# Performance work log

Hardware: AMD Instinct MI355X
Metric: run time of the kernel (lower is better)

## Reference

```python
import jax, jax.numpy as jnp
import numpy as np

N, F_IN, HID, H1, NG = 50000, 128, 64, 4, 512
E = 800000


def setup_inputs() -> dict:
    key = jax.random.key(0)
    ks = jax.random.split(key, 16)
    x = jax.random.normal(ks[0], (N, F_IN), dtype=jnp.float32)
    edge_index = jax.random.randint(ks[1], (2, E), 0, N, dtype=jnp.int64)
    batch = jnp.sort(jax.random.randint(ks[2], (N,), 0, NG, dtype=jnp.int64))
    s = 0.05
    W1 = jax.random.normal(ks[3], (F_IN, H1 * HID), dtype=jnp.float32) * s
    a_src1 = jax.random.normal(ks[4], (H1, HID), dtype=jnp.float32) * s
    a_dst1 = jax.random.normal(ks[5], (H1, HID), dtype=jnp.float32) * s
    b1 = jnp.zeros((H1 * HID,), dtype=jnp.float32)
    W2 = jax.random.normal(ks[6], (H1 * HID, HID), dtype=jnp.float32) * s
    a_src2 = jax.random.normal(ks[7], (1, HID), dtype=jnp.float32) * s
    a_dst2 = jax.random.normal(ks[8], (1, HID), dtype=jnp.float32) * s
    b2 = jnp.zeros((HID,), dtype=jnp.float32)
    Wc = jax.random.normal(ks[9], (HID, 2), dtype=jnp.float32) * s
    bc = jnp.zeros((2,), dtype=jnp.float32)
    return dict(x=x, edge_index=edge_index, batch=batch, W1=W1, a_src1=a_src1,
                a_dst1=a_dst1, b1=b1, W2=W2, a_src2=a_src2, a_dst2=a_dst2,
                b2=b2, Wc=Wc, bc=bc)


def gat_layer(x, W, a_src, a_dst, bias, src, dst, n):
    # PyG GATConv: h = x @ W per head; e_ij = LeakyReLU(a_src.h_j + a_dst.h_i),
    # softmax over incoming edges of each dst node, then scatter-add aggregate.
    H, D = a_src.shape
    h = (x @ W).reshape(n, H, D)                       # [N,H,D]
    asrc = jnp.einsum('nhd,hd->nh', h, a_src)          # [N,H]
    adst = jnp.einsum('nhd,hd->nh', h, a_dst)
    e = jax.nn.leaky_relu(asrc[src] + adst[dst], 0.2)  # [E,H]
    m = jax.lax.stop_gradient(jax.ops.segment_max(e, dst, num_segments=n))
    p = jnp.exp(e - m[dst])
    s = jax.ops.segment_sum(p, dst, num_segments=n)
    alpha = p / (s[dst] + 1e-16)                       # [E,H]
    out = jax.ops.segment_sum(alpha[:, :, None] * h[src], dst, num_segments=n)
    return out.reshape(n, H * D) + bias


def reference(x, edge_index, batch, W1, a_src1, a_dst1, b1, W2, a_src2, a_dst2, b2, Wc, bc):
    n = x.shape[0]
    loops = jnp.arange(n, dtype=edge_index.dtype)
    src = jnp.concatenate([edge_index[0], loops])  # add self-loops (PyG default)
    dst = jnp.concatenate([edge_index[1], loops])
    h = jax.nn.relu(gat_layer(x, W1, a_src1, a_dst1, b1, src, dst, n))
    h = jax.nn.relu(gat_layer(h, W2, a_src2, a_dst2, b2, src, dst, n))
    # global mean pool over graphs
    ng = NG
    sums = jax.ops.segment_sum(h, batch, num_segments=ng)
    cnts = jax.ops.segment_sum(jnp.ones((n,), h.dtype), batch, num_segments=ng)
    pooled = sums / jnp.maximum(cnts, 1.0)[:, None]
    logits = pooled @ Wc + bc
    return jax.nn.log_softmax(logits, axis=1)
```

## Files before the change

kernel.cpp:

```cpp
#include <hip/hip_runtime.h>
#include <hip/hip_bf16.h>
#include <cstddef>
#include <cstdint>

#define FIN   128
#define HID   64
#define H1    4
#define NGRAPH 512
#define BCAP  8192
#define PREB  512

typedef short bf16x8 __attribute__((ext_vector_type(8)));
typedef float f32x4  __attribute__((ext_vector_type(4)));

#if defined(__has_builtin)
#if __has_builtin(__builtin_amdgcn_cvt_f32_fp8) && __has_builtin(__builtin_amdgcn_cvt_pk_fp8_f32)
#define HAVE_HW_FP8 1
#endif
#endif

__device__ __forceinline__ float wave_reduce_sum(float v) {
  #pragma unroll
  for (int off = 32; off > 0; off >>= 1) v += __shfl_down(v, off, 64);
  return v;
}

__device__ __forceinline__ float leaky02(float x) {
  return x > 0.0f ? x : 0.2f * x;
}

__device__ __forceinline__ unsigned short f2bf(float f) {
  union { float f; unsigned int i; } v; v.f = f;
  unsigned int b = v.i;
  return (unsigned short)((b + 0x7FFFu + ((b >> 16) & 1u)) >> 16);
}

#ifndef HAVE_HW_FP8
__device__ __forceinline__ unsigned char f2fp8_1(float f) {
  unsigned int u = __float_as_uint(f);
  unsigned int s = u >> 31;
  u &= 0x7fffffffu;
  if (u > 0x43e00000u) u = 0x43e00000u;
  unsigned int b = u + (0x0007FFFFu + ((u >> 20) & 1u));
  int e = (int)(b >> 23) - 127;
  unsigned int m = (b >> 20) & 7u;
  unsigned char o;
  if (e < -9) o = 0;
  else if (e < -6) { int sh = -6 - e; o = (unsigned char)((8u | m) >> sh); }
  else if (e > 8) o = 0x7e;
  else o = (unsigned char)(((e + 7) << 3) | m);
  return o | (unsigned char)(s << 7);
}
__device__ __forceinline__ float fp8tof_1(unsigned char b) {
  unsigned int s = b >> 7, e = (b >> 3) & 15u, m = b & 7u;
  float v = (e == 0) ? (float)m * 0.001953125f
                     : (float)(8u + m) * __uint_as_float((117u + e) << 23);
  return s ? -v : v;
}
#endif

__device__ __forceinline__ unsigned char f2fp8(float f) {
#ifdef HAVE_HW_FP8
  return (unsigned char)(__builtin_amdgcn_cvt_pk_fp8_f32(f, f, 0u, false) & 0xffu);
#else
  return f2fp8_1(f);
#endif
}
__device__ __forceinline__ float fp8dec(unsigned int w, int i) {
#ifdef HAVE_HW_FP8
  switch (i) {
    case 0: return __builtin_amdgcn_cvt_f32_fp8(w, 0);
    case 1: return __builtin_amdgcn_cvt_f32_fp8(w, 1);
    case 2: return __builtin_amdgcn_cvt_f32_fp8(w, 2);
    default: return __builtin_amdgcn_cvt_f32_fp8(w, 3);
  }
#else
  return fp8tof_1((unsigned char)((w >> (8 * i)) & 0xffu));
#endif
}

__global__ __launch_bounds__(256)
void pre_kernel(const float* __restrict__ W1, const float* __restrict__ W2,
                unsigned short* __restrict__ W1T, unsigned short* __restrict__ W2T,
                const int* __restrict__ dst, int* __restrict__ bucketCnt,
                const int* __restrict__ batch, int* __restrict__ gstart,
                int* __restrict__ gend, int E, int N, int nbuck) {
  __shared__ int lh[256];
  int tid = threadIdx.x;
  lh[tid] = 0;
  __syncthreads();
  int stride = gridDim.x * 256;
  int t0 = blockIdx.x * 256 + tid;
  for (int i = t0; i < E; i += stride)
    atomicAdd(&lh[dst[i] >> 8], 1);
  for (int i = t0; i < N; i += stride) {
    int g = batch[i];
    if (i == 0 || batch[i - 1] != g) gstart[g] = i;
    if (i == N - 1 || batch[i + 1] != g) gend[g] = i + 1;
  }
  for (int u = t0; u < 256 * 128; u += stride) {
    int n = u >> 7, k = u & 127;
    W1T[u] = f2bf(W1[(size_t)k * 256 + n]);
  }
  for (int u = t0; u < 64 * 256; u += stride) {
    int n = u >> 8, k = u & 255;
    W2T[u] = f2bf(W2[(size_t)k * 64 + n]);
  }
  __syncthreads();
  if (tid < nbuck && lh[tid] > 0) atomicAdd(&bucketCnt[tid], lh[tid]);
}

#define P3K 16
__global__ __launch_bounds__(256)
void bpart_kernel(const int* __restrict__ src, const int* __restrict__ dst,
                  int* __restrict__ bucketFill, unsigned int* __restrict__ bucketBuf,
                  int E, int nbuck) {
  __shared__ int lhist[256];
  __shared__ int lbase[256];
  int tid = threadIdx.x;
  int chunk = 256 * P3K;
  for (int start = blockIdx.x * chunk; start < E; start += gridDim.x * chunk) {
    lhist[tid] = 0;
    __syncthreads();
    int mybuck[P3K]; unsigned int mypack[P3K]; int myrank[P3K];
    #pragma unroll
    for (int k = 0; k < P3K; k++) {
      int i = start + k * 256 + tid;
      if (i < E) {
        int d = dst[i];
        int b = d >> 8;
        mybuck[k] = b;
        mypack[k] = (unsigned int)src[i] | ((unsigned int)(d & 255) << 16);
        myrank[k] = atomicAdd(&lhist[b], 1);
      } else mybuck[k] = -1;
    }
    __syncthreads();
    if (tid < nbuck) lbase[tid] = (lhist[tid] > 0) ? atomicAdd(&bucketFill[tid], lhist[tid]) : 0;
    __syncthreads();
    #pragma unroll
    for (int k = 0; k < P3K; k++) {
      if (mybuck[k] >= 0) {
        int b = mybuck[k];
        int pos = lbase[b] + myrank[k];
        if (pos < BCAP) bucketBuf[((size_t)b << 13) + pos] = mypack[k];
      }
    }
    __syncthreads();
  }
}

__global__ __launch_bounds__(256)
void bbuild_kernel(const unsigned int* __restrict__ bucketBuf, const int* __restrict__ bucketCnt,
                   int* __restrict__ rowstart, int* __restrict__ rowend,
                   unsigned short* __restrict__ csr, int N) {
  __shared__ int ldeg[256];
  __shared__ int lscan[256];
  __shared__ int lfill[256];
  int b = blockIdx.x;
  int tid = threadIdx.x;
  int r0 = b << 13;
  int cnt = bucketCnt[b]; if (cnt > BCAP) cnt = BCAP;
  int nb0 = b << 8;
  ldeg[tid] = 0;
  __syncthreads();
  for (int j = tid; j < cnt; j += 256)
    atomicAdd(&ldeg[bucketBuf[r0 + j] >> 16], 1);
  __syncthreads();
  int v = ldeg[tid];
  lscan[tid] = v;
  __syncthreads();
  for (int off = 1; off < 256; off <<= 1) {
    int u = (tid >= off) ? lscan[tid - off] : 0;
    __syncthreads();
    lscan[tid] += u;
    __syncthreads();
  }
  int excl = lscan[tid] - v;
  lfill[tid] = excl;
  if (nb0 + tid < N) {
    rowstart[nb0 + tid] = r0 + excl;
    rowend[nb0 + tid]   = r0 + excl + v;
  }
  __syncthreads();
  for (int j = tid; j < cnt; j += 256) {
    unsigned int p = bucketBuf[r0 + j];
    int pos = r0 + atomicAdd(&lfill[p >> 16], 1);
    csr[pos] = (unsigned short)(p & 0xffffu);
  }
}

__global__ __launch_bounds__(256)
void gemm1_kernel(const float* __restrict__ X, const unsigned short* __restrict__ W1T,
                  unsigned char* __restrict__ h1f8,
                  const float* __restrict__ a_src, const float* __restrict__ a_dst,
                  float* __restrict__ asv, float* __restrict__ adv, int N) {
  __shared__ unsigned short As[64][136];
  __shared__ unsigned short Bs[256][40];
  int t = threadIdx.x;
  int w = t >> 6, lane = t & 63;
  int quad = lane >> 4, l16 = lane & 15;
  int blockRow = blockIdx.x * 64;

  {
    int node = t >> 2, kp = (t & 3) * 32;
    int gn = blockRow + node; if (gn >= N) gn = N - 1;
    const float4* xp = (const float4*)(X + (size_t)gn * 128 + kp);
    #pragma unroll
    for (int i = 0; i < 4; i++) {
      float4 va = xp[2 * i], vb = xp[2 * i + 1];
      union { unsigned short u[8]; uint4 v; } r;
      r.u[0] = f2bf(va.x); r.u[1] = f2bf(va.y); r.u[2] = f2bf(va.z); r.u[3] = f2bf(va.w);
      r.u[4] = f2bf(vb.x); r.u[5] = f2bf(vb.y); r.u[6] = f2bf(vb.z); r.u[7] = f2bf(vb.w);
      *(uint4*)&As[node][kp + i * 8] = r.v;
    }
  }

  f32x4 acc[4][4];
  #pragma unroll
  for (int i = 0; i < 4; i++)
    #pragma unroll
    for (int j = 0; j < 4; j++) acc[i][j] = (f32x4){0.f, 0.f, 0.f, 0.f};

  for (int kc = 0; kc < FIN; kc += 32) {
    {
      const unsigned short* wp = W1T + (size_t)t * 128 + kc;
      #pragma unroll
      for (int i = 0; i < 4; i++) {
        uint4 v = *(const uint4*)(wp + i * 8);
        *(uint4*)&Bs[t][i * 8] = v;
      }
    }
    __syncthreads();
    bf16x8 af[4], bfr[4];
    #pragma unroll
    for (int mt = 0; mt < 4; mt++)
      af[mt] = *(const bf16x8*)&As[mt * 16 + l16][kc + quad * 8];
    #pragma unroll
    for (int nt = 0; nt < 4; nt++)
      bfr[nt] = *(const bf16x8*)&Bs[w * 64 + nt * 16 + l16][quad * 8];
    #pragma unroll
    for (int mt = 0; mt < 4; mt++)
      #pragma unroll
      for (int nt = 0; nt < 4; nt++)
        acc[mt][nt] = __builtin_amdgcn_mfma_f32_16x16x32_bf16(af[mt], bfr[nt], acc[mt][nt], 0, 0, 0);
    __syncthreads();
  }

  float a_s[4], a_d[4];
  #pragma unroll
  for (int nt = 0; nt < 4; nt++) {
    a_s[nt] = a_src[w * 64 + nt * 16 + l16];
    a_d[nt] = a_dst[w * 64 + nt * 16 + l16];
  }
  #pragma unroll
  for (int mt = 0; mt < 4; mt++) {
    #pragma unroll
    for (int reg = 0; reg < 4; reg++) {
      int node = blockRow + mt * 16 + quad * 4 + reg;
      bool ok = node < N;
      float ps = 0.0f, pd = 0.0f;
      #pragma unroll
      for (int nt = 0; nt < 4; nt++) {
        float v = acc[mt][nt][reg];
        ps = fmaf(v, a_s[nt], ps);
        pd = fmaf(v, a_d[nt], pd);
        if (ok) h1f8[(size_t)node * 256 + w * 64 + nt * 16 + l16] = f2fp8(v);
      }
      #pragma unroll
      for (int off = 8; off > 0; off >>= 1) {
        ps += __shfl_xor(ps, off, 16);
        pd += __shfl_xor(pd, off, 16);
      }
      if (l16 == 0 && ok) {
        asv[(size_t)node * 4 + w] = ps;
        adv[(size_t)node * 4 + w] = pd;
      }
    }
  }
}

__global__ __launch_bounds__(256)
void gemm2_kernel(const unsigned short* __restrict__ out1b, const unsigned short* __restrict__ W2T,
                  unsigned char* __restrict__ h2f8,
                  const float* __restrict__ a_src, const float* __restrict__ a_dst,
                  float* __restrict__ asv, float* __restrict__ adv, int N) {
  __shared__ unsigned short As[64][40];
  __shared__ unsigned short Bs[64][40];
  int t = threadIdx.x;
  int w = t >> 6, lane = t & 63;
  int quad = lane >> 4, l16 = lane & 15;
  int blockRow = blockIdx.x * 64;

  f32x4 acc[4];
  #pragma unroll
  for (int j = 0; j < 4; j++) acc[j] = (f32x4){0.f, 0.f, 0.f, 0.f};

  int nodeS = t >> 2, koff = (t & 3) * 8;
  int gnS = blockRow + nodeS; if (gnS >= N) gnS = N - 1;

  for (int kc = 0; kc < 256; kc += 32) {
    {
      uint4 va = *(const uint4*)(out1b + (size_t)gnS * 256 + kc + koff);
      *(uint4*)&As[nodeS][koff] = va;
      uint4 vb = *(const uint4*)(W2T + (size_t)nodeS * 256 + kc + koff);
      *(uint4*)&Bs[nodeS][koff] = vb;
    }
    __syncthreads();
    bf16x8 af = *(const bf16x8*)&As[w * 16 + l16][quad * 8];
    #pragma unroll
    for (int nt = 0; nt < 4; nt++) {
      bf16x8 bfr = *(const bf16x8*)&Bs[nt * 16 + l16][quad * 8];
      acc[nt] = __builtin_amdgcn_mfma_f32_16x16x32_bf16(af, bfr, acc[nt], 0, 0, 0);
    }
    __syncthreads();
  }

  float a_s[4], a_d[4];
  #pragma unroll
  for (int nt = 0; nt < 4; nt++) {
    a_s[nt] = a_src[nt * 16 + l16];
    a_d[nt] = a_dst[nt * 16 + l16];
  }
  #pragma unroll
  for (int reg = 0; reg < 4; reg++) {
    int node = blockRow + w * 16 + quad * 4 + reg;
    bool ok = node < N;
    float ps = 0.0f, pd = 0.0f;
    #pragma unroll
    for (int nt = 0; nt < 4; nt++) {
      float v = acc[nt][reg];
      ps = fmaf(v, a_s[nt], ps);
      pd = fmaf(v, a_d[nt], pd);
      if (ok) h2f8[(size_t)node * 64 + nt * 16 + l16] = f2fp8(v);
    }
    #pragma unroll
    for (int off = 8; off > 0; off >>= 1) {
      ps += __shfl_xor(ps, off, 16);
      pd += __shfl_xor(pd, off, 16);
    }
    if (l16 == 0 && ok) { asv[node] = ps; adv[node] = pd; }
  }
}

__global__ __launch_bounds__(256)
void agg1_kernel(const unsigned char* __restrict__ h1f8, const int* __restrict__ rowstart,
                 const int* __restrict__ rowend, const unsigned short* __restrict__ csr,
                 const float* __restrict__ asv, const float* __restrict__ adv,
                 const float* __restrict__ b1, unsigned short* __restrict__ out1b, int N) {
  __shared__ int   sbuf[4][64];
  __shared__ float pbuf[4][4][68];
  int wv   = threadIdx.x >> 6;
  int lane = threadIdx.x & 63;
  int n = blockIdx.x * 4 + wv;
  if (n >= N) return;
  int r0 = rowstart[n], r1 = rowend[n];
  float4 ad = *(const float4*)(adv + (size_t)n * 4);
  float4 asn = *(const float4*)(asv + (size_t)n * 4);
  int hsel = lane >> 4;

  float es0 = leaky02(asn.x + ad.x);
  float es1 = leaky02(asn.y + ad.y);
  float es2 = leaky02(asn.z + ad.z);
  float es3 = leaky02(asn.w + ad.w);
  float esel = hsel == 0 ? es0 : (hsel == 1 ? es1 : (hsel == 2 ? es2 : es3));

  float q0 = 0, q1 = 0, q2 = 0, q3 = 0;
  float a0 = 0, a1 = 0, a2 = 0, a3 = 0;

  for (int base = r0; base < r1; base += 64) {
    int j = base + lane;
    int cnt = min(64, r1 - base);
    if (j < r1) {
      int s = csr[j];
      float4 as = *(const float4*)(asv + (size_t)s * 4);
      sbuf[wv][lane] = s;
      float p0 = __expf(leaky02(as.x + ad.x));
      float p1 = __expf(leaky02(as.y + ad.y));
      float p2 = __expf(leaky02(as.z + ad.z));
      float p3 = __expf(leaky02(as.w + ad.w));
      pbuf[wv][0][lane] = p0;
      pbuf[wv][1][lane] = p1;
      pbuf[wv][2][lane] = p2;
      pbuf[wv][3][lane] = p3;
      q0 += p0; q1 += p1; q2 += p2; q3 += p3;
    }
    __threadfence_block();

    int c = 0;
    for (; c + 4 <= cnt; c += 4) {
      int4 sv = *(const int4*)&sbuf[wv][c];
      int sc0 = __builtin_amdgcn_readfirstlane(sv.x);
      int sc1 = __builtin_amdgcn_readfirstlane(sv.y);
      int sc2 = __builtin_amdgcn_readfirstlane(sv.z);
      int sc3 = __builtin_amdgcn_readfirstlane(sv.w);
      unsigned int hw0 = *((const unsigned int*)(h1f8 + ((size_t)sc0 << 8)) + lane);
      unsigned int hw1 = *((const unsigned int*)(h1f8 + ((size_t)sc1 << 8)) + lane);
      unsigned int hw2 = *((const unsigned int*)(h1f8 + ((size_t)sc2 << 8)) + lane);
      unsigned int hw3 = *((const unsigned int*)(h1f8 + ((size_t)sc3 << 8)) + lane);
      float4 pv = *(const float4*)&pbuf[wv][hsel][c];
      a0 = fmaf(pv.x, fp8dec(hw0, 0), a0);
      a1 = fmaf(pv.x, fp8dec(hw0, 1), a1);
      a2 = fmaf(pv.x, fp8dec(hw0, 2), a2);
      a3 = fmaf(pv.x, fp8dec(hw0, 3), a3);
      a0 = fmaf(pv.y, fp8dec(hw1, 0), a0);
      a1 = fmaf(pv.y, fp8dec(hw1, 1), a1);
      a2 = fmaf(pv.y, fp8dec(hw1, 2), a2);
      a3 = fmaf(pv.y, fp8dec(hw1, 3), a3);
      a0 = fmaf(pv.z, fp8dec(hw2, 0), a0);
      a1 = fmaf(pv.z, fp8dec(hw2, 1), a1);
      a2 = fmaf(pv.z, fp8dec(hw2, 2), a2);
      a3 = fmaf(pv.z, fp8dec(hw2, 3), a3);
      a0 = fmaf(pv.w, fp8dec(hw3, 0), a0);
      a1 = fmaf(pv.w, fp8dec(hw3, 1), a1);
      a2 = fmaf(pv.w, fp8dec(hw3, 2), a2);
      a3 = fmaf(pv.w, fp8dec(hw3, 3), a3);
    }
    for (; c < cnt; c++) {
      int sc = __builtin_amdgcn_readfirstlane(sbuf[wv][c]);
      float psel = pbuf[wv][hsel][c];
      unsigned int hw = *((const unsigned int*)(h1f8 + ((size_t)sc << 8)) + lane);
      a0 = fmaf(psel, fp8dec(hw, 0), a0);
      a1 = fmaf(psel, fp8dec(hw, 1), a1);
      a2 = fmaf(psel, fp8dec(hw, 2), a2);
      a3 = fmaf(psel, fp8dec(hw, 3), a3);
    }
    __threadfence_block();
  }

  #pragma unroll
  for (int off = 32; off > 0; off >>= 1) {
    q0 += __shfl_xor(q0, off, 64);
    q1 += __shfl_xor(q1, off, 64);
    q2 += __shfl_xor(q2, off, 64);
    q3 += __shfl_xor(q3, off, 64);
  }
  float ssum = hsel == 0 ? q0 : (hsel == 1 ? q1 : (hsel == 2 ? q2 : q3));

  {
    float psel = __expf(esel);
    ssum += psel;
    unsigned int hw = *((const unsigned int*)(h1f8 + ((size_t)n << 8)) + lane);
    a0 = fmaf(psel, fp8dec(hw, 0), a0);
    a1 = fmaf(psel, fp8dec(hw, 1), a1);
    a2 = fmaf(psel, fp8dec(hw, 2), a2);
    a3 = fmaf(psel, fp8dec(hw, 3), a3);
  }

  float inv = 1.0f / (ssum + 1e-16f);
  int d0 = lane * 4;
  float4 bv = *(const float4*)(b1 + d0);
  float v0 = a0 * inv + bv.x;
  float v1 = a1 * inv + bv.y;
  float v2 = a2 * inv + bv.z;
  float v3 = a3 * inv + bv.w;
  ushort4 o;
  o.x = f2bf(v0 > 0 ? v0 : 0.0f);
  o.y = f2bf(v1 > 0 ? v1 : 0.0f);
  o.z = f2bf(v2 > 0 ? v2 : 0.0f);
  o.w = f2bf(v3 > 0 ? v3 : 0.0f);
  *(ushort4*)(out1b + (size_t)n * 256 + d0) = o;
}

__global__ __launch_bounds__(256)
void agg2_kernel(const unsigned char* __restrict__ h2f8, const int* __restrict__ rowstart,
                 const int* __restrict__ rowend, const unsigned short* __restrict__ csr,
                 const float* __restrict__ asv, const float* __restrict__ adv,
                 const float* __restrict__ b2, float* __restrict__ h2out, int N) {
  __shared__ int   sbuf[4][64];
  __shared__ float pbuf[4][64];
  int wv   = threadIdx.x >> 6;
  int lane = threadIdx.x & 63;
  int quad = lane >> 4, l16 = lane & 15;
  int n = blockIdx.x * 4 + wv;
  if (n >= N) return;
  int r0 = rowstart[n], r1 = rowend[n];
  float ad = adv[n];
  float eself = leaky02(asv[n] + ad);
  float q = 0.0f;
  float a0 = 0, a1 = 0, a2 = 0, a3 = 0;

  for (int base = r0; base < r1; base += 64) {
    int j = base + lane;
    int cnt = min(64, r1 - base);
    if (j < r1) {
      int s = csr[j];
      sbuf[wv][lane] = s;
      float p = __expf(leaky02(asv[s] + ad));
      pbuf[wv][lane] = p;
      q += p;
    }
    __threadfence_block();

    int c = 0;
    for (; c + 8 <= cnt; c += 8) {
      int scA = sbuf[wv][c + quad];
      int scB = sbuf[wv][c + 4 + quad];
      float pA = pbuf[wv][c + quad];
      float pB = pbuf[wv][c + 4 + quad];
      unsigned int hwA = *((const unsigned int*)(h2f8 + ((size_t)scA << 6)) + l16);
      unsigned int hwB = *((const unsigned int*)(h2f8 + ((size_t)scB << 6)) + l16);
      a0 = fmaf(pA, fp8dec(hwA, 0), a0);
      a1 = fmaf(pA, fp8dec(hwA, 1), a1);
      a2 = fmaf(pA, fp8dec(hwA, 2), a2);
      a3 = fmaf(pA, fp8dec(hwA, 3), a3);
      a0 = fmaf(pB, fp8dec(hwB, 0), a0);
      a1 = fmaf(pB, fp8dec(hwB, 1), a1);
      a2 = fmaf(pB, fp8dec(hwB, 2), a2);
      a3 = fmaf(pB, fp8dec(hwB, 3), a3);
    }
    for (; c + 4 <= cnt; c += 4) {
      int sc = sbuf[wv][c + quad];
      float p1 = pbuf[wv][c + quad];
      unsigned int hw = *((const unsigned int*)(h2f8 + ((size_t)sc << 6)) + l16);
      a0 = fmaf(p1, fp8dec(hw, 0), a0);
      a1 = fmaf(p1, fp8dec(hw, 1), a1);
      a2 = fmaf(p1, fp8dec(hw, 2), a2);
      a3 = fmaf(p1, fp8dec(hw, 3), a3);
    }
    int rem = cnt - c;
    if (quad < rem) {
      int sc = sbuf[wv][c + quad];
      float p1 = pbuf[wv][c + quad];
      unsigned int hw = *((const unsigned int*)(h2f8 + ((size_t)sc << 6)) + l16);
      a0 = fmaf(p1, fp8dec(hw, 0), a0);
      a1 = fmaf(p1, fp8dec(hw, 1), a1);
      a2 = fmaf(p1, fp8dec(hw, 2), a2);
      a3 = fmaf(p1, fp8dec(hw, 3), a3);
    }
    __threadfence_block();
  }

  #pragma unroll
  for (int off = 32; off > 0; off >>= 1) q += __shfl_xor(q, off, 64);
  #pragma unroll
  for (int off = 16; off <= 32; off <<= 1) {
    a0 += __shfl_xor(a0, off, 64);
    a1 += __shfl_xor(a1, off, 64);
    a2 += __shfl_xor(a2, off, 64);
    a3 += __shfl_xor(a3, off, 64);
  }
  float ssum = q;

  {
    float p = __expf(eself);
    ssum += p;
    unsigned int hw = *((const unsigned int*)(h2f8 + ((size_t)n << 6)) + l16);
    a0 = fmaf(p, fp8dec(hw, 0), a0);
    a1 = fmaf(p, fp8dec(hw, 1), a1);
    a2 = fmaf(p, fp8dec(hw, 2), a2);
    a3 = fmaf(p, fp8dec(hw, 3), a3);
  }

  if (quad == 0) {
    float inv = 1.0f / (ssum + 1e-16f);
    float4 bv = *(const float4*)(b2 + l16 * 4);
    float4 o;
    float v0 = a0 * inv + bv.x;
    float v1 = a1 * inv + bv.y;
    float v2 = a2 * inv + bv.z;
    float v3 = a3 * inv + bv.w;
    o.x = v0 > 0 ? v0 : 0.0f;
    o.y = v1 > 0 ? v1 : 0.0f;
    o.z = v2 > 0 ? v2 : 0.0f;
    o.w = v3 > 0 ? v3 : 0.0f;
    *(float4*)(h2out + (size_t)n * 64 + l16 * 4) = o;
  }
}

__global__ __launch_bounds__(256)
void pool_kernel(const float* __restrict__ h2, const int* __restrict__ gstart,
                 const int* __restrict__ gend, const float* __restrict__ Wc,
                 const float* __restrict__ bc, float* __restrict__ out) {
  int g = blockIdx.x;
  int w = threadIdx.x >> 6, lane = threadIdx.x & 63;
  int s = gstart[g], e = gend[g];
  float acc = 0.0f;
  for (int n = s + w; n < e; n += 4) acc += h2[(size_t)n * 64 + lane];
  __shared__ float red[4][64];
  red[w][lane] = acc;
  __syncthreads();
  if (w == 0) {
    float v = red[0][lane] + red[1][lane] + red[2][lane] + red[3][lane];
    float pooled = (e > s) ? v / (float)(e - s) : 0.0f;
    float l0 = wave_reduce_sum(pooled * Wc[lane * 2 + 0]);
    float l1 = wave_reduce_sum(pooled * Wc[lane * 2 + 1]);
    if (lane == 0) {
      l0 += bc[0]; l1 += bc[1];
      float mx = fmaxf(l0, l1);
      float lse = mx + logf(__expf(l0 - mx) + __expf(l1 - mx));
      out[g * 2 + 0] = l0 - lse;
      out[g * 2 + 1] = l1 - lse;
    }
  }
}

extern "C" void kernel_launch(void* const* d_in, const int* in_sizes, int n_in,
                              void* d_out, int out_size, void* d_ws, size_t ws_size,
                              hipStream_t stream) {
  const float* x      = (const float*)d_in[0];
  const int*   ei     = (const int*)d_in[1];
  const int*   batch  = (const int*)d_in[2];
  const float* W1     = (const float*)d_in[3];
  const float* a_src1 = (const float*)d_in[4];
  const float* a_dst1 = (const float*)d_in[5];
  const float* b1     = (const float*)d_in[6];
  const float* W2     = (const float*)d_in[7];
  const float* a_src2 = (const float*)d_in[8];
  const float* a_dst2 = (const float*)d_in[9];
  const float* b2     = (const float*)d_in[10];
  const float* Wc     = (const float*)d_in[11];
  const float* bc     = (const float*)d_in[12];
  float* out = (float*)d_out;

  const int N = in_sizes[0] / FIN;
  const int E = in_sizes[1] / 2;
  const int* srcArr = ei;
  const int* dstArr = ei + E;
  const int nbuck = (N + 255) >> 8;

  char* base = (char*)d_ws;
  size_t off = 0;
  auto alloc = [&](size_t bytes) -> void* {
    void* p = base + off;
    off = (off + bytes + 255) & ~(size_t)255;
    return p;
  };
  unsigned short* W1T  = (unsigned short*)alloc((size_t)256 * 128 * 2);
  unsigned short* W2T  = (unsigned short*)alloc((size_t)64 * 256 * 2);
  unsigned char*  h1f8 = (unsigned char*)alloc((size_t)N * 256);
  unsigned short* out1b= (unsigned short*)alloc((size_t)N * 256 * 2);
  unsigned char*  h2f8 = (unsigned char*)alloc((size_t)N * 64);
  float* h2    = (float*)alloc((size_t)N * 64 * 4);
  float* asv1  = (float*)alloc((size_t)N * 4 * 4);
  float* adv1  = (float*)alloc((size_t)N * 4 * 4);
  float* asv2  = (float*)alloc((size_t)N * 4);
  float* adv2  = (float*)alloc((size_t)N * 4);
  int*   bucketCnt = (int*)alloc(256 * 4);
  int*   bucketFill= (int*)alloc(256 * 4);
  int*   gstart= (int*)alloc(NGRAPH * 4);
  int*   gend  = (int*)alloc(NGRAPH * 4);
  size_t zspan = (size_t)((char*)gend + NGRAPH * 4 - (char*)bucketCnt);
  int*   rowstart = (int*)alloc((size_t)N * 4);
  int*   rowend   = (int*)alloc((size_t)N * 4);
  unsigned int* bucketBuf = (unsigned int*)alloc((size_t)nbuck * BCAP * 4);
  unsigned short* csr = (unsigned short*)alloc((size_t)nbuck * BCAP * 2);
  (void)ws_size; (void)n_in; (void)out_size;

  int gridWv = (N + 3) / 4;
  int gridG  = (N + 63) / 64;
  int gridP3 = (E + 256 * P3K - 1) / (256 * P3K);

  hipMemsetAsync(bucketCnt, 0, zspan, stream);
  pre_kernel<<<PREB, 256, 0, stream>>>(W1, W2, W1T, W2T, dstArr, bucketCnt,
                                       batch, gstart, gend, E, N, nbuck);
  bpart_kernel<<<gridP3, 256, 0, stream>>>(srcArr, dstArr, bucketFill, bucketBuf, E, nbuck);
  bbuild_kernel<<<nbuck, 256, 0, stream>>>(bucketBuf, bucketCnt, rowstart, rowend, csr, N);

  gemm1_kernel<<<gridG, 256, 0, stream>>>(x, W1T, h1f8, a_src1, a_dst1, asv1, adv1, N);
  agg1_kernel<<<gridWv, 256, 0, stream>>>(h1f8, rowstart, rowend, csr, asv1, adv1, b1, out1b, N);

  gemm2_kernel<<<gridG, 256, 0, stream>>>(out1b, W2T, h2f8, a_src2, a_dst2, asv2, adv2, N);
  agg2_kernel<<<gridWv, 256, 0, stream>>>(h2f8, rowstart, rowend, csr, asv2, adv2, b2, h2, N);

  pool_kernel<<<NGRAPH, 256, 0, stream>>>(h2, gstart, gend, Wc, bc, out);
}
```

Baseline: 241.0 us.

## Fold pre-pass into bucket partition kernel and unroll agg1 gather by eight

Removes the separate pre_kernel that histogrammed destination buckets, and moves its weight transposes and graph-boundary detection into bpart_kernel. bbuild now takes bucket counts from the atomic fill counters bpart already keeps, so one full read of dst and one launch go away. The agg1 inner gather loop also gets an 8-wide unrolled step ahead of the 4-wide one, putting more independent fp8 row loads in flight. The costs are higher register pressure in agg1 and some extra serial work in every bpart block.

```diff
diff --git a/kernel.cpp b/kernel.cpp
--- a/kernel.cpp
+++ b/kernel.cpp
@@ -8,7 +8,6 @@
 #define H1    4
 #define NGRAPH 512
 #define BCAP  8192
-#define PREB  512
 
 typedef short bf16x8 __attribute__((ext_vector_type(8)));
 typedef float f32x4  __attribute__((ext_vector_type(4)));
@@ -79,45 +78,33 @@
 #endif
 }
 
+#define P3K 16
 __global__ __launch_bounds__(256)
-void pre_kernel(const float* __restrict__ W1, const float* __restrict__ W2,
-                unsigned short* __restrict__ W1T, unsigned short* __restrict__ W2T,
-                const int* __restrict__ dst, int* __restrict__ bucketCnt,
-                const int* __restrict__ batch, int* __restrict__ gstart,
-                int* __restrict__ gend, int E, int N, int nbuck) {
-  __shared__ int lh[256];
+void bpart_kernel(const int* __restrict__ src, const int* __restrict__ dst,
+                  int* __restrict__ bucketFill, unsigned int* __restrict__ bucketBuf,
+                  const float* __restrict__ W1, const float* __restrict__ W2,
+                  unsigned short* __restrict__ W1T, unsigned short* __restrict__ W2T,
+                  const int* __restrict__ batch, int* __restrict__ gstart,
+                  int* __restrict__ gend, int E, int N, int nbuck) {
   int tid = threadIdx.x;
-  lh[tid] = 0;
-  __syncthreads();
   int stride = gridDim.x * 256;
   int t0 = blockIdx.x * 256 + tid;
-  for (int i = t0; i < E; i += stride)
-    atomicAdd(&lh[dst[i] >> 8], 1);
+  for (int u = t0; u < 256 * 128; u += stride) {
+    int n = u >> 7, k = u & 127;
+    W1T[u] = f2bf(W1[(size_t)k * 256 + n]);
+  }
+  for (int u = t0; u < 64 * 256; u += stride) {
+    int n = u >> 8, k = u & 255;
+    W2T[u] = f2bf(W2[(size_t)k * 64 + n]);
+  }
   for (int i = t0; i < N; i += stride) {
     int g = batch[i];
     if (i == 0 || batch[i - 1] != g) gstart[g] = i;
     if (i == N - 1 || batch[i + 1] != g) gend[g] = i + 1;
   }
-  for (int u = t0; u < 256 * 128; u += stride) {
-    int n = u >> 7, k = u & 127;
-    W1T[u] = f2bf(W1[(size_t)k * 256 + n]);
-  }
-  for (int u = t0; u < 64 * 256; u += stride) {
-    int n = u >> 8, k = u & 255;
-    W2T[u] = f2bf(W2[(size_t)k * 64 + n]);
-  }
-  __syncthreads();
-  if (tid < nbuck && lh[tid] > 0) atomicAdd(&bucketCnt[tid], lh[tid]);
-}
-
-#define P3K 16
-__global__ __launch_bounds__(256)
-void bpart_kernel(const int* __restrict__ src, const int* __restrict__ dst,
-                  int* __restrict__ bucketFill, unsigned int* __restrict__ bucketBuf,
-                  int E, int nbuck) {
+
   __shared__ int lhist[256];
   __shared__ int lbase[256];
-  int tid = threadIdx.x;
   int chunk = 256 * P3K;
   for (int start = blockIdx.x * chunk; start < E; start += gridDim.x * chunk) {
     lhist[tid] = 0;
@@ -150,7 +137,7 @@
 }
 
 __global__ __launch_bounds__(256)
-void bbuild_kernel(const unsigned int* __restrict__ bucketBuf, const int* __restrict__ bucketCnt,
+void bbuild_kernel(const unsigned int* __restrict__ bucketBuf, const int* __restrict__ bucketFill,
                    int* __restrict__ rowstart, int* __restrict__ rowend,
                    unsigned short* __restrict__ csr, int N) {
   __shared__ int ldeg[256];
@@ -159,7 +146,7 @@
   int b = blockIdx.x;
   int tid = threadIdx.x;
   int r0 = b << 13;
-  int cnt = bucketCnt[b]; if (cnt > BCAP) cnt = BCAP;
+  int cnt = bucketFill[b]; if (cnt > BCAP) cnt = BCAP;
   int nb0 = b << 8;
   ldeg[tid] = 0;
   __syncthreads();
@@ -387,6 +374,60 @@
     __threadfence_block();
 
     int c = 0;
+    for (; c + 8 <= cnt; c += 8) {
+      int4 sva = *(const int4*)&sbuf[wv][c];
+      int4 svb = *(const int4*)&sbuf[wv][c + 4];
+      int sc0 = __builtin_amdgcn_readfirstlane(sva.x);
+      int sc1 = __builtin_amdgcn_readfirstlane(sva.y);
+      int sc2 = __builtin_amdgcn_readfirstlane(sva.z);
+      int sc3 = __builtin_amdgcn_readfirstlane(sva.w);
+      int sc4 = __builtin_amdgcn_readfirstlane(svb.x);
+      int sc5 = __builtin_amdgcn_readfirstlane(svb.y);
+      int sc6 = __builtin_amdgcn_readfirstlane(svb.z);
+      int sc7 = __builtin_amdgcn_readfirstlane(svb.w);
+      unsigned int hw0 = *((const unsigned int*)(h1f8 + ((size_t)sc0 << 8)) + lane);
+      unsigned int hw1 = *((const unsigned int*)(h1f8 + ((size_t)sc1 << 8)) + lane);
+      unsigned int hw2 = *((const unsigned int*)(h1f8 + ((size_t)sc2 << 8)) + lane);
+      unsigned int hw3 = *((const unsigned int*)(h1f8 + ((size_t)sc3 << 8)) + lane);
+      unsigned int hw4 = *((const unsigned int*)(h1f8 + ((size_t)sc4 << 8)) + lane);
+      unsigned int hw5 = *((const unsigned int*)(h1f8 + ((size_t)sc5 << 8)) + lane);
+      unsigned int hw6 = *((const unsigned int*)(h1f8 + ((size_t)sc6 << 8)) + lane);
+      unsigned int hw7 = *((const unsigned int*)(h1f8 + ((size_t)sc7 << 8)) + lane);
+      float4 pva = *(const float4*)&pbuf[wv][hsel][c];
+      float4 pvb = *(const float4*)&pbuf[wv][hsel][c + 4];
+      a0 = fmaf(pva.x, fp8dec(hw0, 0), a0);
+      a1 = fmaf(pva.x, fp8dec(hw0, 1), a1);
+      a2 = fmaf(pva.x, fp8dec(hw0, 2), a2);
+      a3 = fmaf(pva.x, fp8dec(hw0, 3), a3);
+      a0 = fmaf(pva.y, fp8dec(hw1, 0), a0);
+      a1 = fmaf(pva.y, fp8dec(hw1, 1), a1);
+      a2 = fmaf(pva.y, fp8dec(hw1, 2), a2);
+      a3 = fmaf(pva.y, fp8dec(hw1, 3), a3);
+      a0 = fmaf(pva.z, fp8dec(hw2, 0), a0);
+      a1 = fmaf(pva.z, fp8dec(hw2, 1), a1);
+      a2 = fmaf(pva.z, fp8dec(hw2, 2), a2);
+      a3 = fmaf(pva.z, fp8dec(hw2, 3), a3);
+      a0 = fmaf(pva.w, fp8dec(hw3, 0), a0);
+      a1 = fmaf(pva.w, fp8dec(hw3, 1), a1);
+      a2 = fmaf(pva.w, fp8dec(hw3, 2), a2);
+      a3 = fmaf(pva.w, fp8dec(hw3, 3), a3);
+      a0 = fmaf(pvb.x, fp8dec(hw4, 0), a0);
+      a1 = fmaf(pvb.x, fp8dec(hw4, 1), a1);
+      a2 = fmaf(pvb.x, fp8dec(hw4, 2), a2);
+      a3 = fmaf(pvb.x, fp8dec(hw4, 3), a3);
+      a0 = fmaf(pvb.y, fp8dec(hw5, 0), a0);
+      a1 = fmaf(pvb.y, fp8dec(hw5, 1), a1);
+      a2 = fmaf(pvb.y, fp8dec(hw5, 2), a2);
+      a3 = fmaf(pvb.y, fp8dec(hw5, 3), a3);
+      a0 = fmaf(pvb.z, fp8dec(hw6, 0), a0);
+      a1 = fmaf(pvb.z, fp8dec(hw6, 1), a1);
+      a2 = fmaf(pvb.z, fp8dec(hw6, 2), a2);
+      a3 = fmaf(pvb.z, fp8dec(hw6, 3), a3);
+      a0 = fmaf(pvb.w, fp8dec(hw7, 0), a0);
+      a1 = fmaf(pvb.w, fp8dec(hw7, 1), a1);
+      a2 = fmaf(pvb.w, fp8dec(hw7, 2), a2);
+      a3 = fmaf(pvb.w, fp8dec(hw7, 3), a3);
+    }
     for (; c + 4 <= cnt; c += 4) {
       int4 sv = *(const int4*)&sbuf[wv][c];
       int sc0 = __builtin_amdgcn_readfirstlane(sv.x);
@@ -635,11 +676,10 @@
   float* adv1  = (float*)alloc((size_t)N * 4 * 4);
   float* asv2  = (float*)alloc((size_t)N * 4);
   float* adv2  = (float*)alloc((size_t)N * 4);
-  int*   bucketCnt = (int*)alloc(256 * 4);
   int*   bucketFill= (int*)alloc(256 * 4);
   int*   gstart= (int*)alloc(NGRAPH * 4);
   int*   gend  = (int*)alloc(NGRAPH * 4);
-  size_t zspan = (size_t)((char*)gend + NGRAPH * 4 - (char*)bucketCnt);
+  size_t zspan = (size_t)((char*)gend + NGRAPH * 4 - (char*)bucketFill);
   int*   rowstart = (int*)alloc((size_t)N * 4);
   int*   rowend   = (int*)alloc((size_t)N * 4);
   unsigned int* bucketBuf = (unsigned int*)alloc((size_t)nbuck * BCAP * 4);
@@ -650,11 +690,11 @@
   int gridG  = (N + 63) / 64;
   int gridP3 = (E + 256 * P3K - 1) / (256 * P3K);
 
-  hipMemsetAsync(bucketCnt, 0, zspan, stream);
-  pre_kernel<<<PREB, 256, 0, stream>>>(W1, W2, W1T, W2T, dstArr, bucketCnt,
-                                       batch, gstart, gend, E, N, nbuck);
-  bpart_kernel<<<gridP3, 256, 0, stream>>>(srcArr, dstArr, bucketFill, bucketBuf, E, nbuck);
-  bbuild_kernel<<<nbuck, 256, 0, stream>>>(bucketBuf, bucketCnt, rowstart, rowend, csr, N);
+  hipMemsetAsync(bucketFill, 0, zspan, stream);
+  bpart_kernel<<<gridP3, 256, 0, stream>>>(srcArr, dstArr, bucketFill, bucketBuf,
+                                           W1, W2, W1T, W2T, batch, gstart, gend,
+                                           E, N, nbuck);
+  bbuild_kernel<<<nbuck, 256, 0, stream>>>(bucketBuf, bucketFill, rowstart, rowend, csr, N);
 
   gemm1_kernel<<<gridG, 256, 0, stream>>>(x, W1T, h1f8, a_src1, a_dst1, asv1, adv1, N);
   agg1_kernel<<<gridWv, 256, 0, stream>>>(h1f8, rowstart, rowend, csr, asv1, adv1, b1, out1b, N);
```

Measured after the change: 229.0 us. 1.05x faster.
